# Kernel tuning notes

Hardware: AMD Instinct MI355X
Metric: run time of the kernel (lower is better)

Reference implementation:

```python
import jax, jax.numpy as jnp
import numpy as np

N_NODES = 50000
N_EDGES = 600000
D = 128


def setup_inputs() -> dict:
    key = jax.random.key(0)
    ks = jax.random.split(key, 8)
    x = jax.random.normal(ks[0], (N_NODES, D), dtype=jnp.float32)
    edge_index = jax.random.randint(ks[1], (2, N_EDGES), 0, N_NODES, dtype=jnp.int64)
    s = 1.0 / np.sqrt(D)
    W_l1 = jax.random.uniform(ks[2], (D, D), jnp.float32, -s, s)
    W_r1 = jax.random.uniform(ks[3], (D, D), jnp.float32, -s, s)
    b1 = jnp.zeros((D,), jnp.float32)
    W_l2 = jax.random.uniform(ks[4], (D, D), jnp.float32, -s, s)
    W_r2 = jax.random.uniform(ks[5], (D, D), jnp.float32, -s, s)
    b2 = jnp.zeros((D,), jnp.float32)
    return {"x": x, "edge_index": edge_index, "W_l1": W_l1, "W_r1": W_r1,
            "b1": b1, "W_l2": W_l2, "W_r2": W_r2, "b2": b2}


def _sage_conv(x, src, dst, W_l, W_r, b):
    # mean aggregation over incoming edges (src -> dst), PyG SAGEConv semantics
    n = x.shape[0]
    msg = x[src]                                               # [E, D] gather
    agg = jax.ops.segment_sum(msg, dst, num_segments=n)        # [N, D] scatter-add
    cnt = jax.ops.segment_sum(jnp.ones((src.shape[0],), x.dtype), dst, num_segments=n)
    mean = agg / jnp.maximum(cnt, 1.0)[:, None]
    return mean @ W_l + x @ W_r + b


def reference(x, edge_index, W_l1, W_r1, b1, W_l2, W_r2, b2):
    src, dst = edge_index[0], edge_index[1]
    h = jax.nn.relu(_sage_conv(x, src, dst, W_l1, W_r1, b1))
    out = _sage_conv(h, src, dst, W_l2, W_r2, b2)
    return out
```

## Files before the change

### kernel.cpp

```cpp
#include <hip/hip_runtime.h>
#include <hip/hip_bf16.h>

#define N_NODES 50000
#define N_EDGES 600000
#define D 128
#define K2 256
#define MAXDEG 64

#define CVT_BLOCKS   (N_NODES * 16 / 256)
#define PREPW_BLOCKS (2 * D * K2 / 256)
#define PREP_GRID (CVT_BLOCKS + PREPW_BLOCKS)

typedef __bf16 bf16x8 __attribute__((ext_vector_type(8)));
typedef float  f32x16 __attribute__((ext_vector_type(16)));

__device__ __forceinline__ unsigned short f32_to_bf16_rne(float f) {
    unsigned int u = __builtin_bit_cast(unsigned int, f);
    unsigned int r = (u + 0x7fffu + ((u >> 16) & 1u)) >> 16;
    return (unsigned short)r;
}
__device__ __forceinline__ unsigned pk2(float lo, float hi) {
    return (unsigned)f32_to_bf16_rne(lo) | ((unsigned)f32_to_bf16_rne(hi) << 16);
}
__device__ __forceinline__ float bfl(unsigned int u) { return __builtin_bit_cast(float, u << 16); }
__device__ __forceinline__ float bfh(unsigned int u) { return __builtin_bit_cast(float, u & 0xffff0000u); }

__global__ __launch_bounds__(256) void prep_kernel(
    const float* __restrict__ x, const int* __restrict__ ei,
    const float* __restrict__ Wl1, const float* __restrict__ Wr1,
    const float* __restrict__ Wl2, const float* __restrict__ Wr2,
    unsigned short* __restrict__ A0, unsigned short* __restrict__ WT,
    int* __restrict__ counts, int* __restrict__ slots)
{
    const int b = blockIdx.x;
    if (b < CVT_BLOCKS) {
        int idx = b * 256 + threadIdx.x;
        int e4 = idx * 4;
        int4 s4 = {0,0,0,0}, d4 = {0,0,0,0};
        const bool doE = e4 < N_EDGES;
        if (doE) {
            s4 = *(const int4*)(ei + e4);
            d4 = *(const int4*)(ei + N_EDGES + e4);
        }
        int node = idx >> 4, g = idx & 15;
        const float4* xp = (const float4*)(x + (size_t)node * D + g * 8);
        float4 v0 = xp[0], v1 = xp[1];
        if (doE) {
            int p0 = atomicAdd(&counts[d4.x], 1);
            int p1 = atomicAdd(&counts[d4.y], 1);
            int p2 = atomicAdd(&counts[d4.z], 1);
            int p3 = atomicAdd(&counts[d4.w], 1);
            if (p0 < MAXDEG) slots[(size_t)d4.x * MAXDEG + p0] = s4.x;
            if (p1 < MAXDEG) slots[(size_t)d4.y * MAXDEG + p1] = s4.y;
            if (p2 < MAXDEG) slots[(size_t)d4.z * MAXDEG + p2] = s4.z;
            if (p3 < MAXDEG) slots[(size_t)d4.w * MAXDEG + p3] = s4.w;
        }
        uint4 o;
        o.x = pk2(v0.x, v0.y); o.y = pk2(v0.z, v0.w);
        o.z = pk2(v1.x, v1.y); o.w = pk2(v1.z, v1.w);
        ((uint4*)A0)[(size_t)node * 16 + g] = o;
    } else {
        int idx = (b - CVT_BLOCKS) * 256 + threadIdx.x;
        int layer = idx >> 15, rem = idx & 32767;
        int n = rem >> 8, k = rem & 255;
        const float* Wl = layer ? Wl2 : Wl1;
        const float* Wr = layer ? Wr2 : Wr1;
        float v = (k < D) ? Wl[k * D + n] : Wr[(k - D) * D + n];
        WT[((size_t)layer << 15) + n * K2 + k] = f32_to_bf16_rne(v);
    }
}

template <bool RELU, bool OUT_BF16>
__global__ __launch_bounds__(256, 4) void layer_kernel(
    const unsigned short* __restrict__ Xin,
    const int* __restrict__ counts, const int* __restrict__ slots,
    const unsigned short* __restrict__ WT,
    const float* __restrict__ bias,
    unsigned short* __restrict__ Hout,
    float* __restrict__ outf)
{
    __shared__ uint4 As4[32 * 33];
    const int tid = threadIdx.x;
    const int lane = tid & 63;
    const int wv = tid >> 6;
    const int base = blockIdx.x * 32;
    const int g = lane >> 4;
    const int u = lane & 15;
    const uint4* X4 = (const uint4*)Xin;
    const int nodeb = base + wv * 8;

    const int n0 = nodeb + g;
    const int n1 = nodeb + 4 + g;
    const bool ok0 = n0 < N_NODES, ok1 = n1 < N_NODES;

    int cnt0 = 0, cnt1 = 0;
    if (ok0) cnt0 = counts[n0];
    if (ok1) cnt1 = counts[n1];

    int sreg[2][4];
    #pragma unroll
    for (int r = 0; r < 4; ++r) {
        sreg[0][r] = ok0 ? slots[(size_t)n0 * MAXDEG + r * 16 + u] : 0;
        sreg[1][r] = ok1 ? slots[(size_t)n1 * MAXDEG + r * 16 + u] : 0;
    }

    uint4 xv0 = {0u,0u,0u,0u}, xv1 = {0u,0u,0u,0u};
    if (ok0) xv0 = X4[(size_t)n0 * 16 + u];
    if (ok1) xv1 = X4[(size_t)n1 * 16 + u];

    cnt0 = cnt0 > MAXDEG ? MAXDEG : cnt0;
    cnt1 = cnt1 > MAXDEG ? MAXDEG : cnt1;

    #pragma unroll
    for (int s = 0; s < 2; ++s) {
        const int m = wv * 8 + s * 4 + g;
        const int cnt = s ? cnt1 : cnt0;
        float a0 = 0.f, a1 = 0.f, a2 = 0.f, a3 = 0.f;
        float a4 = 0.f, a5 = 0.f, a6 = 0.f, a7 = 0.f;

        #pragma unroll
        for (int r = 0; r < 4; ++r) {
            if (r == 0 || __any(cnt > r * 16)) {
                int idxv[16];
                #pragma unroll
                for (int e = 0; e < 16; ++e) {
                    int t = __shfl(sreg[s][r], g * 16 + e, 64);
                    idxv[e] = (r * 16 + e < cnt) ? t : 0;
                }
                uint4 vv[16];
                #pragma unroll
                for (int e = 0; e < 16; ++e) {
                    const uint4* p = X4 + (size_t)idxv[e] * 16 + u;
                    asm volatile("global_load_dwordx4 %0, %1, off"
                                 : "=v"(vv[e]) : "v"(p) : "memory");
                }
                asm volatile("s_waitcnt vmcnt(0)" ::: "memory");
                __builtin_amdgcn_sched_barrier(0);
                #pragma unroll
                for (int e = 0; e < 16; ++e) {
                    if (r * 16 + e < cnt) {
                        a0 += bfl(vv[e].x); a1 += bfh(vv[e].x);
                        a2 += bfl(vv[e].y); a3 += bfh(vv[e].y);
                        a4 += bfl(vv[e].z); a5 += bfh(vv[e].z);
                        a6 += bfl(vv[e].w); a7 += bfh(vv[e].w);
                    }
                }
            }
        }

        const float inv = 1.0f / fmaxf((float)cnt, 1.0f);
        uint4 o;
        o.x = pk2(a0 * inv, a1 * inv); o.y = pk2(a2 * inv, a3 * inv);
        o.z = pk2(a4 * inv, a5 * inv); o.w = pk2(a6 * inv, a7 * inv);
        As4[u * 33 + m] = o;
    }

    As4[(16 + u) * 33 + (wv * 8 + g)]     = xv0;
    As4[(16 + u) * 33 + (wv * 8 + 4 + g)] = xv1;

    __syncthreads();

    const int m = lane & 31;
    const int kg = lane >> 5;
    const int col = wv * 32 + m;
    const uint4* bp = (const uint4*)(WT + (size_t)col * K2 + kg * 8);
    const bf16x8* afrag = (const bf16x8*)As4;

    f32x16 acc = {};
    #pragma unroll
    for (int s = 0; s < 16; ++s) {
        bf16x8 a = afrag[(s * 2 + kg) * 33 + m];
        bf16x8 b = __builtin_bit_cast(bf16x8, bp[s * 2]);
        acc = __builtin_amdgcn_mfma_f32_32x32x16_bf16(a, b, acc, 0, 0, 0);
    }

    const float bc = bias[col];
    const int halfadd = kg * 4;
    #pragma unroll
    for (int r = 0; r < 16; ++r) {
        int rw = base + (r & 3) + 8 * (r >> 2) + halfadd;
        if (rw < N_NODES) {
            float v = acc[r] + bc;
            if (RELU) v = fmaxf(v, 0.0f);
            if (OUT_BF16) Hout[(size_t)rw * D + col] = f32_to_bf16_rne(v);
            else outf[(size_t)rw * D + col] = v;
        }
    }
}

extern "C" void kernel_launch(void* const* d_in, const int* in_sizes, int n_in,
                              void* d_out, int out_size, void* d_ws, size_t ws_size,
                              hipStream_t stream) {
    const float* x   = (const float*)d_in[0];
    const int*   ei  = (const int*)d_in[1];
    const float* Wl1 = (const float*)d_in[2];
    const float* Wr1 = (const float*)d_in[3];
    const float* b1  = (const float*)d_in[4];
    const float* Wl2 = (const float*)d_in[5];
    const float* Wr2 = (const float*)d_in[6];
    const float* b2  = (const float*)d_in[7];
    float* out = (float*)d_out;

    unsigned short* A0 = (unsigned short*)d_ws;
    unsigned short* A1 = A0 + (size_t)N_NODES * D;
    unsigned short* WT = A1 + (size_t)N_NODES * D;
    int* counts = (int*)(WT + 2 * D * K2);
    int* slots  = counts + N_NODES;

    const int layerBlocks = (N_NODES + 31) / 32;

    hipMemsetAsync(counts, 0, N_NODES * sizeof(int), stream);
    prep_kernel<<<PREP_GRID, 256, 0, stream>>>(x, ei, Wl1, Wr1, Wl2, Wr2, A0, WT, counts, slots);

    layer_kernel<true, true><<<layerBlocks, 256, 0, stream>>>(
        A0, counts, slots, WT, b1, A1, nullptr);
    layer_kernel<false, false><<<layerBlocks, 256, 0, stream>>>(
        A1, counts, slots, WT + (size_t)D * K2, b2, nullptr, out);
}
```

Before: 208.8 us.

## Fuse prep and both layers into one cooperative persistent kernel

Replaces the memset, prep kernel and two layer launches with a single cooperative kernel. It zeroes counts, converts inputs and weights, builds the adjacency, then runs both layers, with grid.sync between phases and an atomic tile counter for dynamic scheduling. This removes launch gaps and inter-kernel boundaries. In exchange it adds grid-wide barriers, serialises the edge-building phase after conversion, and costs an atomic plus two block barriers per tile.

```diff
diff --git a/kernel.cpp b/kernel.cpp
--- a/kernel.cpp
+++ b/kernel.cpp
@@ -1,15 +1,16 @@
 #include <hip/hip_runtime.h>
 #include <hip/hip_bf16.h>
+#include <hip/hip_cooperative_groups.h>
+
+namespace cg = cooperative_groups;
 
 #define N_NODES 50000
 #define N_EDGES 600000
 #define D 128
 #define K2 256
 #define MAXDEG 64
-
-#define CVT_BLOCKS   (N_NODES * 16 / 256)
-#define PREPW_BLOCKS (2 * D * K2 / 256)
-#define PREP_GRID (CVT_BLOCKS + PREPW_BLOCKS)
+#define LAYER_TILES ((N_NODES + 31) / 32)
+#define MAX_GRID 1024
 
 typedef __bf16 bf16x8 __attribute__((ext_vector_type(8)));
 typedef float  f32x16 __attribute__((ext_vector_type(16)));
@@ -25,53 +26,9 @@
 __device__ __forceinline__ float bfl(unsigned int u) { return __builtin_bit_cast(float, u << 16); }
 __device__ __forceinline__ float bfh(unsigned int u) { return __builtin_bit_cast(float, u & 0xffff0000u); }
 
-__global__ __launch_bounds__(256) void prep_kernel(
-    const float* __restrict__ x, const int* __restrict__ ei,
-    const float* __restrict__ Wl1, const float* __restrict__ Wr1,
-    const float* __restrict__ Wl2, const float* __restrict__ Wr2,
-    unsigned short* __restrict__ A0, unsigned short* __restrict__ WT,
-    int* __restrict__ counts, int* __restrict__ slots)
-{
-    const int b = blockIdx.x;
-    if (b < CVT_BLOCKS) {
-        int idx = b * 256 + threadIdx.x;
-        int e4 = idx * 4;
-        int4 s4 = {0,0,0,0}, d4 = {0,0,0,0};
-        const bool doE = e4 < N_EDGES;
-        if (doE) {
-            s4 = *(const int4*)(ei + e4);
-            d4 = *(const int4*)(ei + N_EDGES + e4);
-        }
-        int node = idx >> 4, g = idx & 15;
-        const float4* xp = (const float4*)(x + (size_t)node * D + g * 8);
-        float4 v0 = xp[0], v1 = xp[1];
-        if (doE) {
-            int p0 = atomicAdd(&counts[d4.x], 1);
-            int p1 = atomicAdd(&counts[d4.y], 1);
-            int p2 = atomicAdd(&counts[d4.z], 1);
-            int p3 = atomicAdd(&counts[d4.w], 1);
-            if (p0 < MAXDEG) slots[(size_t)d4.x * MAXDEG + p0] = s4.x;
-            if (p1 < MAXDEG) slots[(size_t)d4.y * MAXDEG + p1] = s4.y;
-            if (p2 < MAXDEG) slots[(size_t)d4.z * MAXDEG + p2] = s4.z;
-            if (p3 < MAXDEG) slots[(size_t)d4.w * MAXDEG + p3] = s4.w;
-        }
-        uint4 o;
-        o.x = pk2(v0.x, v0.y); o.y = pk2(v0.z, v0.w);
-        o.z = pk2(v1.x, v1.y); o.w = pk2(v1.z, v1.w);
-        ((uint4*)A0)[(size_t)node * 16 + g] = o;
-    } else {
-        int idx = (b - CVT_BLOCKS) * 256 + threadIdx.x;
-        int layer = idx >> 15, rem = idx & 32767;
-        int n = rem >> 8, k = rem & 255;
-        const float* Wl = layer ? Wl2 : Wl1;
-        const float* Wr = layer ? Wr2 : Wr1;
-        float v = (k < D) ? Wl[k * D + n] : Wr[(k - D) * D + n];
-        WT[((size_t)layer << 15) + n * K2 + k] = f32_to_bf16_rne(v);
-    }
-}
-
 template <bool RELU, bool OUT_BF16>
-__global__ __launch_bounds__(256, 4) void layer_kernel(
+__device__ __forceinline__ void layer_tile(
+    int base, uint4* As4,
     const unsigned short* __restrict__ Xin,
     const int* __restrict__ counts, const int* __restrict__ slots,
     const unsigned short* __restrict__ WT,
@@ -79,11 +36,9 @@
     unsigned short* __restrict__ Hout,
     float* __restrict__ outf)
 {
-    __shared__ uint4 As4[32 * 33];
     const int tid = threadIdx.x;
     const int lane = tid & 63;
     const int wv = tid >> 6;
-    const int base = blockIdx.x * 32;
     const int g = lane >> 4;
     const int u = lane & 15;
     const uint4* X4 = (const uint4*)Xin;
@@ -188,6 +143,87 @@
     }
 }
 
+template <bool RELU, bool OUT_BF16>
+__device__ __forceinline__ void layer_phase(
+    uint4* As4, int* tile_s, int* ctr,
+    const unsigned short* Xin, const int* counts, const int* slots,
+    const unsigned short* WT, const float* bias,
+    unsigned short* Hout, float* outf)
+{
+    while (true) {
+        if (threadIdx.x == 0) *tile_s = atomicAdd(ctr, 1);
+        __syncthreads();
+        int tile = *tile_s;
+        if (tile >= LAYER_TILES) break;
+        layer_tile<RELU, OUT_BF16>(tile * 32, As4, Xin, counts, slots, WT,
+                                   bias, Hout, outf);
+        __syncthreads();
+    }
+}
+
+__global__ __launch_bounds__(256, 4) void fused_kernel(
+    const float* __restrict__ x, const int* __restrict__ ei,
+    const float* __restrict__ Wl1, const float* __restrict__ Wr1,
+    const float* __restrict__ b1,
+    const float* __restrict__ Wl2, const float* __restrict__ Wr2,
+    const float* __restrict__ b2,
+    unsigned short* __restrict__ A0, unsigned short* __restrict__ A1,
+    unsigned short* __restrict__ WT,
+    int* __restrict__ counts, int* __restrict__ slots,
+    int* __restrict__ tctr, float* __restrict__ out)
+{
+    __shared__ uint4 As4[32 * 33];
+    __shared__ int tile_s;
+    cg::grid_group grid = cg::this_grid();
+    const int gsz = gridDim.x * 256;
+    const int gt = blockIdx.x * 256 + threadIdx.x;
+
+    for (int i = gt; i < N_NODES; i += gsz) counts[i] = 0;
+    if (gt == 0) { tctr[0] = 0; tctr[1] = 0; }
+    for (int i = gt; i < 2 * D * K2; i += gsz) {
+        int layer = i >> 15, rem = i & 32767;
+        int n = rem >> 8, k = rem & 255;
+        const float* Wl = layer ? Wl2 : Wl1;
+        const float* Wr = layer ? Wr2 : Wr1;
+        float v = (k < D) ? Wl[k * D + n] : Wr[(k - D) * D + n];
+        WT[((size_t)layer << 15) + n * K2 + k] = f32_to_bf16_rne(v);
+    }
+    for (int i = gt; i < N_NODES * 16; i += gsz) {
+        int node = i >> 4, g = i & 15;
+        const float4* xp = (const float4*)(x + (size_t)node * D + g * 8);
+        float4 v0 = xp[0], v1 = xp[1];
+        uint4 o;
+        o.x = pk2(v0.x, v0.y); o.y = pk2(v0.z, v0.w);
+        o.z = pk2(v1.x, v1.y); o.w = pk2(v1.z, v1.w);
+        ((uint4*)A0)[(size_t)node * 16 + g] = o;
+    }
+    __threadfence();
+    grid.sync();
+
+    for (int e4 = gt * 4; e4 < N_EDGES; e4 += gsz * 4) {
+        int4 s4 = *(const int4*)(ei + e4);
+        int4 d4 = *(const int4*)(ei + N_EDGES + e4);
+        int p0 = atomicAdd(&counts[d4.x], 1);
+        int p1 = atomicAdd(&counts[d4.y], 1);
+        int p2 = atomicAdd(&counts[d4.z], 1);
+        int p3 = atomicAdd(&counts[d4.w], 1);
+        if (p0 < MAXDEG) slots[(size_t)d4.x * MAXDEG + p0] = s4.x;
+        if (p1 < MAXDEG) slots[(size_t)d4.y * MAXDEG + p1] = s4.y;
+        if (p2 < MAXDEG) slots[(size_t)d4.z * MAXDEG + p2] = s4.z;
+        if (p3 < MAXDEG) slots[(size_t)d4.w * MAXDEG + p3] = s4.w;
+    }
+    __threadfence();
+    grid.sync();
+
+    layer_phase<true, true>(As4, &tile_s, &tctr[0], A0, counts, slots,
+                            WT, b1, A1, nullptr);
+    __threadfence();
+    grid.sync();
+
+    layer_phase<false, false>(As4, &tile_s, &tctr[1], A1, counts, slots,
+                              WT + (size_t)D * K2, b2, nullptr, out);
+}
+
 extern "C" void kernel_launch(void* const* d_in, const int* in_sizes, int n_in,
                               void* d_out, int out_size, void* d_ws, size_t ws_size,
                               hipStream_t stream) {
@@ -206,14 +242,19 @@
     unsigned short* WT = A1 + (size_t)N_NODES * D;
     int* counts = (int*)(WT + 2 * D * K2);
     int* slots  = counts + N_NODES;
-
-    const int layerBlocks = (N_NODES + 31) / 32;
-
-    hipMemsetAsync(counts, 0, N_NODES * sizeof(int), stream);
-    prep_kernel<<<PREP_GRID, 256, 0, stream>>>(x, ei, Wl1, Wr1, Wl2, Wr2, A0, WT, counts, slots);
-
-    layer_kernel<true, true><<<layerBlocks, 256, 0, stream>>>(
-        A0, counts, slots, WT, b1, A1, nullptr);
-    layer_kernel<false, false><<<layerBlocks, 256, 0, stream>>>(
-        A1, counts, slots, WT + (size_t)D * K2, b2, nullptr, out);
-}
+    int* tctr   = slots + (size_t)N_NODES * MAXDEG;
+
+    int occ = 4;
+    (void)hipOccupancyMaxActiveBlocksPerMultiprocessor(
+        &occ, reinterpret_cast<const void*>(fused_kernel), 256, 0);
+    if (occ < 1) occ = 1;
+    int grid = occ * 256;
+    if (grid > MAX_GRID) grid = MAX_GRID;
+
+    void* args[] = { (void*)&x, (void*)&ei, (void*)&Wl1, (void*)&Wr1, (void*)&b1,
+                     (void*)&Wl2, (void*)&Wr2, (void*)&b2, (void*)&A0, (void*)&A1,
+                     (void*)&WT, (void*)&counts, (void*)&slots, (void*)&tctr,
+                     (void*)&out };
+    hipLaunchCooperativeKernel(reinterpret_cast<const void*>(fused_kernel),
+                               dim3(grid), dim3(256), args, 0, stream);
+}
```

After: 576.6 us. +176.2%, slower.
